# Kernel optimization log

Measured on AMD Instinct MI355X. Metric: run time of the kernel, lower is better.

## Reference

```python
import jax, jax.numpy as jnp
import numpy as np

N = 100000       # nodes
E = 1600000      # edges
DIM_IN = 128
DIM_H = 256
G = 512          # graphs in batch


def setup_inputs() -> dict:
    key = jax.random.key(0)
    ks = jax.random.split(key, 9)
    x = jax.random.normal(ks[0], (N, DIM_IN), dtype=jnp.float32)
    edge_index = jax.random.randint(ks[1], (2, E), 0, N, dtype=jnp.int32)
    batch = jnp.sort(jax.random.randint(ks[2], (N,), 0, G, dtype=jnp.int32))
    # GCNConv weights (glorot-ish scale) + biases, and linear head
    W1 = jax.random.normal(ks[3], (DIM_IN, DIM_H), dtype=jnp.float32) / np.sqrt(DIM_IN)
    b1 = jnp.zeros((DIM_H,), dtype=jnp.float32)
    W2 = jax.random.normal(ks[4], (DIM_H, DIM_H), dtype=jnp.float32) / np.sqrt(DIM_H)
    b2 = jnp.zeros((DIM_H,), dtype=jnp.float32)
    Wl = jax.random.normal(ks[5], (DIM_H, 1), dtype=jnp.float32) / np.sqrt(DIM_H)
    bl = jnp.zeros((1,), dtype=jnp.float32)
    return {"x": x, "edge_index": edge_index, "batch": batch,
            "W1": W1, "b1": b1, "W2": W2, "b2": b2, "Wl": Wl, "bl": bl}


def _gcn_conv(x, W, b, src, dst, norm):
    # PyG GCNConv: h = x @ W; message = norm_e * h[src]; aggregate at dst; + bias
    h = x @ W                                  # [N, d_out]
    msg = h[src] * norm[:, None]               # [E+N, d_out] edge-gathered
    out = jax.ops.segment_sum(msg, dst, num_segments=N)
    return out + b


def reference(x, edge_index, batch, W1, b1, W2, b2, Wl, bl):
    # add self-loops (PyG GCNConv default)
    loops = jnp.arange(N, dtype=edge_index.dtype)
    src = jnp.concatenate([edge_index[0], loops])   # [E+N]
    dst = jnp.concatenate([edge_index[1], loops])   # [E+N]
    # symmetric normalization: deg counted at dst (incl. self-loops)
    deg = jax.ops.segment_sum(jnp.ones_like(src, dtype=x.dtype), dst, num_segments=N)
    dinv = jax.lax.rsqrt(deg)                       # deg >= 1 due to self-loops
    norm = dinv[src] * dinv[dst]                    # [E+N]

    h = jax.nn.relu(_gcn_conv(x, W1, b1, src, dst, norm))
    h = jax.nn.relu(_gcn_conv(h, W2, b2, src, dst, norm))

    # global_mean_pool over graph ids
    sums = jax.ops.segment_sum(h, batch, num_segments=G)                  # [G, d]
    cnts = jax.ops.segment_sum(jnp.ones((N,), h.dtype), batch, num_segments=G)
    pooled = sums / jnp.maximum(cnts, 1.0)[:, None]

    return pooled @ Wl + bl                                              # [G, 1]
```

## Files before the change

### kernel.cpp

```cpp
#include <hip/hip_runtime.h>
#include <hip/hip_fp16.h>
#include <math.h>

typedef _Float16 f16x8 __attribute__((ext_vector_type(8)));
typedef float f32x4 __attribute__((ext_vector_type(4)));


__global__ void k_init(int* __restrict__ ecnt, int* __restrict__ cursor, int N) {
    int i = blockIdx.x * 256 + threadIdx.x;
    if (i < N) { ecnt[i] = 0; cursor[i] = 0; }
}

__global__ void k_edge_count(const int* __restrict__ dst, int* __restrict__ ecnt, int E) {
    int i = blockIdx.x * 256 + threadIdx.x;
    if (i < E) atomicAdd(&ecnt[dst[i]], 1);
}

__global__ void k_scanA(const int* __restrict__ ecnt, int* __restrict__ bsum, int N) {
    int t = threadIdx.x;
    int base = blockIdx.x * 1024;
    int s = 0;
#pragma unroll
    for (int j = 0; j < 4; ++j) {
        int i = base + j * 256 + t;
        if (i < N) s += ecnt[i];
    }
#pragma unroll
    for (int off = 32; off > 0; off >>= 1) s += __shfl_down(s, off, 64);
    __shared__ int wsum[4];
    if ((t & 63) == 0) wsum[t >> 6] = s;
    __syncthreads();
    if (t == 0) bsum[blockIdx.x] = wsum[0] + wsum[1] + wsum[2] + wsum[3];
}

__global__ void k_scanB(const int* __restrict__ bsum, int* __restrict__ boff, int NB) {
    __shared__ int sh[256];
    int t = threadIdx.x;
    int v = (t < NB) ? bsum[t] : 0;
    sh[t] = v;
    __syncthreads();
    for (int off = 1; off < 256; off <<= 1) {
        int u = (t >= off) ? sh[t - off] : 0;
        __syncthreads();
        sh[t] += u;
        __syncthreads();
    }
    if (t < NB) boff[t] = sh[t] - v;
}

__global__ void k_scanC(const int* __restrict__ ecnt, const int* __restrict__ boff,
                        int* __restrict__ rowstart, float* __restrict__ dinv, int N) {
    int t = threadIdx.x;
    int base = blockIdx.x * 1024 + t * 4;
    int e[4];
    int s = 0;
#pragma unroll
    for (int j = 0; j < 4; ++j) {
        int i = base + j;
        e[j] = (i < N) ? ecnt[i] : 0;
        s += e[j];
    }
    __shared__ int sh[256];
    sh[t] = s;
    __syncthreads();
    for (int off = 1; off < 256; off <<= 1) {
        int u = (t >= off) ? sh[t - off] : 0;
        __syncthreads();
        sh[t] += u;
        __syncthreads();
    }
    int off0 = boff[blockIdx.x] + sh[t] - s;
    int run = 0;
#pragma unroll
    for (int j = 0; j < 4; ++j) {
        int i = base + j;
        if (i < N) {
            rowstart[i] = off0 + run;
            dinv[i] = rsqrtf((float)(e[j] + 1));
        }
        run += e[j];
    }
}

__global__ void k_tail(int* __restrict__ rowstart, int N, int E) {
    rowstart[N] = E;
}

__global__ void k_scatter(const int* __restrict__ src, const int* __restrict__ dst,
                          const int* __restrict__ rowstart, int* __restrict__ cursor,
                          int* __restrict__ ssrc, int E) {
    int i = blockIdx.x * 256 + threadIdx.x;
    if (i < E) {
        int v = dst[i];
        int p = rowstart[v] + atomicAdd(&cursor[v], 1);
        ssrc[p] = src[i];
    }
}

__global__ void k_gstarts(const int* __restrict__ batch, int* __restrict__ gstart, int N, int G) {
    int i = blockIdx.x * 256 + threadIdx.x;
    if (i >= N) return;
    int bi = batch[i];
    int bp = (i == 0) ? -1 : batch[i - 1];
    for (int g = bp + 1; g <= bi; ++g) gstart[g] = i;
    if (i == N - 1) {
        for (int g = bi + 1; g <= G; ++g) gstart[g] = N;
    }
}


__global__ __launch_bounds__(256) void k_cast_f2h(const float* __restrict__ in,
                                                  __half* __restrict__ out, int n4) {
    int i = blockIdx.x * 256 + threadIdx.x;
    if (i >= n4) return;
    float4 v = *(const float4*)(in + (size_t)i * 4);
    __half2 a = __floats2half2_rn(v.x, v.y);
    __half2 b = __floats2half2_rn(v.z, v.w);
    union { __half2 h[2]; float2 f; } u;
    u.h[0] = a; u.h[1] = b;
    *(float2*)(out + (size_t)i * 4) = u.f;
}


__global__ __launch_bounds__(256) void k_wt(const float* __restrict__ W,
                                            _Float16* __restrict__ Wt, int K) {
    int idx = blockIdx.x * 256 + threadIdx.x;
    if (idx >= K * 256) return;
    int c = idx / K, k = idx - c * K;
    Wt[idx] = (_Float16)W[k * 256 + c];
}


__device__ __forceinline__ void acc_h4(float4& acc, float2 raw, float d) {
    union { float2 f; __half2 h[2]; } u;
    u.f = raw;
    float2 p0 = __half22float2(u.h[0]);
    float2 p1 = __half22float2(u.h[1]);
    acc.x = fmaf(p0.x, d, acc.x);
    acc.y = fmaf(p0.y, d, acc.y);
    acc.z = fmaf(p1.x, d, acc.z);
    acc.w = fmaf(p1.y, d, acc.w);
}

__global__ __launch_bounds__(256) void k_agg_in(
    const float* __restrict__ x, const __half* __restrict__ xh,
    const int* __restrict__ rowstart, const int* __restrict__ ssrc,
    const float* __restrict__ dinv, __half* __restrict__ xa_h, int N) {
    int half_id = threadIdx.x >> 5;
    int l = threadIdx.x & 31;
    int v = blockIdx.x * 8 + half_id;
    if (v >= N) return;
    float dv = dinv[v];
    float4 s = *(const float4*)(x + (size_t)v * 128 + l * 4);
    float4 acc = make_float4(s.x * dv, s.y * dv, s.z * dv, s.w * dv);
    int e = rowstart[v], e1 = rowstart[v + 1];
    for (; e + 4 <= e1; e += 4) {
        int u0 = ssrc[e], u1 = ssrc[e + 1], u2 = ssrc[e + 2], u3 = ssrc[e + 3];
        float d0 = dinv[u0], d1 = dinv[u1], d2 = dinv[u2], d3 = dinv[u3];
        float2 m0 = *(const float2*)(xh + (size_t)u0 * 128 + l * 4);
        float2 m1 = *(const float2*)(xh + (size_t)u1 * 128 + l * 4);
        float2 m2 = *(const float2*)(xh + (size_t)u2 * 128 + l * 4);
        float2 m3 = *(const float2*)(xh + (size_t)u3 * 128 + l * 4);
        acc_h4(acc, m0, d0);
        acc_h4(acc, m1, d1);
        acc_h4(acc, m2, d2);
        acc_h4(acc, m3, d3);
    }
    for (; e < e1; ++e) {
        int u = ssrc[e];
        float d = dinv[u];
        float2 m = *(const float2*)(xh + (size_t)u * 128 + l * 4);
        acc_h4(acc, m, d);
    }
    union { __half2 h[2]; float2 f; } uo;
    uo.h[0] = __floats2half2_rn(acc.x * dv, acc.y * dv);
    uo.h[1] = __floats2half2_rn(acc.z * dv, acc.w * dv);
    *(float2*)(xa_h + (size_t)v * 128 + l * 4) = uo.f;
}


__device__ __forceinline__ void acc_h4s(float4& acc, float2 raw) {
    union { float2 f; __half2 h[2]; } u;
    u.f = raw;
    float2 p0 = __half22float2(u.h[0]);
    float2 p1 = __half22float2(u.h[1]);
    acc.x += p0.x; acc.y += p0.y; acc.z += p1.x; acc.w += p1.y;
}

__global__ __launch_bounds__(256) void k_aggregate(
    const __half* __restrict__ hsh, const int* __restrict__ rowstart,
    const int* __restrict__ ssrc, const float* __restrict__ dinv,
    const float* __restrict__ bias, float* __restrict__ out, int N) {
    int w = threadIdx.x >> 6;
    int l = threadIdx.x & 63;
    int v = blockIdx.x * 4 + w;
    if (v >= N) return;
    float4 acc = make_float4(0.f, 0.f, 0.f, 0.f);
    acc_h4s(acc, *(const float2*)(hsh + (size_t)v * 256 + l * 4));
    int e = rowstart[v], e1 = rowstart[v + 1];
    for (; e + 4 <= e1; e += 4) {
        int u0 = ssrc[e], u1 = ssrc[e + 1], u2 = ssrc[e + 2], u3 = ssrc[e + 3];
        float2 m0 = *(const float2*)(hsh + (size_t)u0 * 256 + l * 4);
        float2 m1 = *(const float2*)(hsh + (size_t)u1 * 256 + l * 4);
        float2 m2 = *(const float2*)(hsh + (size_t)u2 * 256 + l * 4);
        float2 m3 = *(const float2*)(hsh + (size_t)u3 * 256 + l * 4);
        acc_h4s(acc, m0);
        acc_h4s(acc, m1);
        acc_h4s(acc, m2);
        acc_h4s(acc, m3);
    }
    for (; e < e1; ++e) {
        int u = ssrc[e];
        acc_h4s(acc, *(const float2*)(hsh + (size_t)u * 256 + l * 4));
    }
    float d = dinv[v];
    float4 b = *(const float4*)(bias + l * 4);
    float4 o;
    o.x = fmaxf(fmaf(acc.x, d, b.x), 0.f);
    o.y = fmaxf(fmaf(acc.y, d, b.y), 0.f);
    o.z = fmaxf(fmaf(acc.z, d, b.z), 0.f);
    o.w = fmaxf(fmaf(acc.w, d, b.w), 0.f);
    *(float4*)(out + (size_t)v * 256 + l * 4) = o;
}


template<int K, int EPI>
__global__ __launch_bounds__(256, 2) void k_gemm_mfma(
    const _Float16* __restrict__ Ah, const _Float16* __restrict__ Wt,
    const float* __restrict__ dinv, const float* __restrict__ bias,
    _Float16* __restrict__ Ch, int Nrows, int nchunks) {
    constexpr int KS = K / 32;
    constexpr int RB = 2 * K;
    constexpr int NLD = 64 * RB / 4096;
    __shared__ _Float16 As[64 * K];

    int tid = threadIdx.x;
    int l = tid & 63;
    int wv = tid >> 6;

    int bc = wv * 64 + (l & 15);
    int bk = (l >> 4) * 8;
    f16x8 breg[4][KS];
#pragma unroll
    for (int ct = 0; ct < 4; ++ct)
#pragma unroll
        for (int ks = 0; ks < KS; ++ks)
            breg[ct][ks] = *(const f16x8*)(Wt + (size_t)(bc + ct * 16) * K + ks * 32 + bk);
    float bb[4];
    if (EPI == 1) {
#pragma unroll
        for (int ct = 0; ct < 4; ++ct) bb[ct] = bias[bc + ct * 16];
    }

    for (int ch = blockIdx.x; ch < nchunks; ch += gridDim.x) {
        int r0 = ch * 64;
#pragma unroll
        for (int i = 0; i < NLD; ++i) {
            int logical = i * 4096 + tid * 16;
            int row = logical / RB;
            int colb = (logical & (RB - 1)) ^ ((row & 7) << 4);
            int grow = r0 + row;
            grow = grow < Nrows ? grow : Nrows - 1;
            const char* src = (const char*)Ah + (size_t)grow * RB + colb;
            char* dst = (char*)As + i * 4096 + wv * 1024;
            __builtin_amdgcn_global_load_lds(
                (const __attribute__((address_space(1))) void*)src,
                (__attribute__((address_space(3))) void*)dst, 16, 0, 0);
        }
        __syncthreads();

#pragma unroll
        for (int rb = 0; rb < 4; ++rb) {
            f32x4 acc[4];
#pragma unroll
            for (int ct = 0; ct < 4; ++ct) acc[ct] = (f32x4){0.f, 0.f, 0.f, 0.f};
            int row = rb * 16 + (l & 15);
#pragma unroll
            for (int ks = 0; ks < KS; ++ks) {
                int lb = (row * RB + ks * 64 + (l >> 4) * 16) ^ ((l & 7) << 4);
                f16x8 a = *(const f16x8*)((const char*)As + lb);
#pragma unroll
                for (int ct = 0; ct < 4; ++ct)
                    acc[ct] = __builtin_amdgcn_mfma_f32_16x16x32_f16(a, breg[ct][ks], acc[ct], 0, 0, 0);
            }
            int rbase = r0 + rb * 16 + (l >> 4) * 4;
#pragma unroll
            for (int j = 0; j < 4; ++j) {
                int r = rbase + j;
                if (r < Nrows) {
                    if (EPI == 0) {
                        float sc = dinv[r];
#pragma unroll
                        for (int ct = 0; ct < 4; ++ct)
                            Ch[(size_t)r * 256 + bc + ct * 16] = (_Float16)(acc[ct][j] * sc);
                    } else {
#pragma unroll
                        for (int ct = 0; ct < 4; ++ct)
                            Ch[(size_t)r * 256 + bc + ct * 16] =
                                (_Float16)fmaxf(acc[ct][j] + bb[ct], 0.f);
                    }
                }
            }
        }
        __syncthreads();
    }
}


__global__ __launch_bounds__(256) void k_pool_head(
    const float* __restrict__ h2, const int* __restrict__ gstart,
    const float* __restrict__ Wl, const float* __restrict__ bl,
    float* __restrict__ out, int G) {
    int g = blockIdx.x;
    int t = threadIdx.x;
    int i0 = gstart[g], i1 = gstart[g + 1];
    float s = 0.f;
    for (int i = i0; i < i1; ++i) s += h2[(size_t)i * 256 + t];
    float cnt = (float)(i1 - i0);
    float pooled = s / fmaxf(cnt, 1.f);
    float v = pooled * Wl[t];
#pragma unroll
    for (int off = 32; off > 0; off >>= 1) v += __shfl_down(v, off, 64);
    __shared__ float red[4];
    if ((t & 63) == 0) red[t >> 6] = v;
    __syncthreads();
    if (t == 0) out[g] = red[0] + red[1] + red[2] + red[3] + bl[0];
}


extern "C" void kernel_launch(void* const* d_in, const int* in_sizes, int n_in,
                              void* d_out, int out_size, void* d_ws, size_t ws_size,
                              hipStream_t stream) {
    const float* x  = (const float*)d_in[0];
    const int* ei   = (const int*)d_in[1];
    const int* batch= (const int*)d_in[2];
    const float* W1 = (const float*)d_in[3];
    const float* b1 = (const float*)d_in[4];
    const float* W2 = (const float*)d_in[5];
    const float* b2 = (const float*)d_in[6];
    const float* Wl = (const float*)d_in[7];
    const float* bl = (const float*)d_in[8];
    float* out = (float*)d_out;

    const int N = in_sizes[2];
    const int E = in_sizes[1] / 2;
    const int G = out_size;

    char* wsp = (char*)d_ws;
    size_t off = 0;
    auto carve = [&](size_t bytes) -> void* {
        void* p = wsp + off;
        off = (off + bytes + 255) & ~(size_t)255;
        return p;
    };
    float* bufA    = (float*)carve((size_t)N * 256 * 4);
    float* bufB    = (float*)carve((size_t)N * 256 * 4);
    float* dinv    = (float*)carve((size_t)N * 4);
    int* ecnt      = (int*)carve((size_t)N * 4);
    int* rowstart  = (int*)carve((size_t)(N + 1) * 4);
    int* cursor    = (int*)carve((size_t)N * 4);
    int* ssrc      = (int*)carve((size_t)E * 4);
    const int NB = (N + 1023) / 1024;
    int* bsum      = (int*)carve((size_t)NB * 4);
    int* boff      = (int*)carve((size_t)NB * 4);
    int* gstart    = (int*)carve((size_t)(G + 1) * 4);
    _Float16* W1t  = (_Float16*)carve((size_t)256 * 128 * 2);
    _Float16* W2t  = (_Float16*)carve((size_t)256 * 256 * 2);
    (void)ws_size;

    __half*    xh   = (__half*)bufA;
    __half*    xa_h = (__half*)((char*)bufA + (size_t)N * 128 * 2);
    _Float16*  h1h  = (_Float16*)((char*)bufA + (size_t)N * 128 * 4);
    _Float16*  hsh  = (_Float16*)bufB;
    float*     h2   = bufA;

    const int* esrc = ei;
    const int* edst = ei + E;

    int nb256 = (N + 255) / 256;
    int eb256 = (E + 255) / 256;
    int nchunks = (N + 63) / 64;

    hipLaunchKernelGGL(k_init, dim3(nb256), dim3(256), 0, stream, ecnt, cursor, N);
    hipLaunchKernelGGL(k_edge_count, dim3(eb256), dim3(256), 0, stream, edst, ecnt, E);
    hipLaunchKernelGGL(k_scanA, dim3(NB), dim3(256), 0, stream, ecnt, bsum, N);
    hipLaunchKernelGGL(k_scanB, dim3(1), dim3(256), 0, stream, bsum, boff, NB);
    hipLaunchKernelGGL(k_scanC, dim3(NB), dim3(256), 0, stream, ecnt, boff, rowstart, dinv, N);
    hipLaunchKernelGGL(k_tail, dim3(1), dim3(1), 0, stream, rowstart, N, E);
    hipLaunchKernelGGL(k_scatter, dim3(eb256), dim3(256), 0, stream, esrc, edst, rowstart, cursor, ssrc, E);
    hipLaunchKernelGGL(k_gstarts, dim3(nb256), dim3(256), 0, stream, batch, gstart, N, G);
    hipLaunchKernelGGL(k_cast_f2h, dim3((N * 32 + 255) / 256), dim3(256), 0, stream,
                       x, xh, N * 32);
    hipLaunchKernelGGL(k_wt, dim3(128), dim3(256), 0, stream, W1, W1t, 128);
    hipLaunchKernelGGL(k_wt, dim3(256), dim3(256), 0, stream, W2, W2t, 256);

    hipLaunchKernelGGL(k_agg_in, dim3((N + 7) / 8), dim3(256), 0, stream,
                       x, xh, rowstart, ssrc, dinv, xa_h, N);
    hipLaunchKernelGGL((k_gemm_mfma<128, 1>), dim3(512), dim3(256), 0, stream,
                       (const _Float16*)xa_h, W1t, (const float*)nullptr, b1, h1h, N, nchunks);
    hipLaunchKernelGGL((k_gemm_mfma<256, 0>), dim3(512), dim3(256), 0, stream,
                       h1h, W2t, dinv, (const float*)nullptr, hsh, N, nchunks);
    hipLaunchKernelGGL(k_aggregate, dim3((N + 3) / 4), dim3(256), 0, stream,
                       (const __half*)hsh, rowstart, ssrc, dinv, b2, h2, N);
    hipLaunchKernelGGL(k_pool_head, dim3(G), dim3(256), 0, stream, h2, gstart, Wl, bl, out, G);
}
```

Measured before the change: 493.2 us.

## Fuse second aggregation with mean pooling, widen gathers, merge tiny kernels

```diff
diff --git a/kernel.cpp b/kernel.cpp
--- a/kernel.cpp
+++ b/kernel.cpp
@@ -12,8 +12,14 @@
 }
 
 __global__ void k_edge_count(const int* __restrict__ dst, int* __restrict__ ecnt, int E) {
-    int i = blockIdx.x * 256 + threadIdx.x;
-    if (i < E) atomicAdd(&ecnt[dst[i]], 1);
+    int j = (blockIdx.x * 256 + threadIdx.x) * 2;
+    if (j + 1 < E) {
+        int2 d = *(const int2*)(dst + j);
+        atomicAdd(&ecnt[d.x], 1);
+        atomicAdd(&ecnt[d.y], 1);
+    } else if (j < E) {
+        atomicAdd(&ecnt[dst[j]], 1);
+    }
 }
 
 __global__ void k_scanA(const int* __restrict__ ecnt, int* __restrict__ bsum, int N) {
@@ -33,7 +39,8 @@
     if (t == 0) bsum[blockIdx.x] = wsum[0] + wsum[1] + wsum[2] + wsum[3];
 }
 
-__global__ void k_scanB(const int* __restrict__ bsum, int* __restrict__ boff, int NB) {
+__global__ void k_scanB(const int* __restrict__ bsum, int* __restrict__ boff, int NB,
+                        int* __restrict__ rowstart, int N, int E) {
     __shared__ int sh[256];
     int t = threadIdx.x;
     int v = (t < NB) ? bsum[t] : 0;
@@ -46,6 +53,7 @@
         __syncthreads();
     }
     if (t < NB) boff[t] = sh[t] - v;
+    if (t == 0) rowstart[N] = E;
 }
 
 __global__ void k_scanC(const int* __restrict__ ecnt, const int* __restrict__ boff,
@@ -82,23 +90,28 @@
     }
 }
 
-__global__ void k_tail(int* __restrict__ rowstart, int N, int E) {
-    rowstart[N] = E;
-}
-
 __global__ void k_scatter(const int* __restrict__ src, const int* __restrict__ dst,
                           const int* __restrict__ rowstart, int* __restrict__ cursor,
                           int* __restrict__ ssrc, int E) {
+    int j = (blockIdx.x * 256 + threadIdx.x) * 2;
+    if (j + 1 < E) {
+        int2 s = *(const int2*)(src + j);
+        int2 d = *(const int2*)(dst + j);
+        int p0 = rowstart[d.x] + atomicAdd(&cursor[d.x], 1);
+        ssrc[p0] = s.x;
+        int p1 = rowstart[d.y] + atomicAdd(&cursor[d.y], 1);
+        ssrc[p1] = s.y;
+    } else if (j < E) {
+        int v = dst[j];
+        int p = rowstart[v] + atomicAdd(&cursor[v], 1);
+        ssrc[p] = src[j];
+    }
+}
+
+__global__ void k_gstarts(const int* __restrict__ batch, int* __restrict__ gstart,
+                          float* __restrict__ pooled, int N, int G) {
     int i = blockIdx.x * 256 + threadIdx.x;
-    if (i < E) {
-        int v = dst[i];
-        int p = rowstart[v] + atomicAdd(&cursor[v], 1);
-        ssrc[p] = src[i];
-    }
-}
-
-__global__ void k_gstarts(const int* __restrict__ batch, int* __restrict__ gstart, int N, int G) {
-    int i = blockIdx.x * 256 + threadIdx.x;
+    if (i < G * 256) pooled[i] = 0.f;
     if (i >= N) return;
     int bi = batch[i];
     int bp = (i == 0) ? -1 : batch[i - 1];
@@ -131,96 +144,115 @@
 }
 
 
-__device__ __forceinline__ void acc_h4(float4& acc, float2 raw, float d) {
-    union { float2 f; __half2 h[2]; } u;
-    u.f = raw;
-    float2 p0 = __half22float2(u.h[0]);
-    float2 p1 = __half22float2(u.h[1]);
-    acc.x = fmaf(p0.x, d, acc.x);
-    acc.y = fmaf(p0.y, d, acc.y);
-    acc.z = fmaf(p1.x, d, acc.z);
-    acc.w = fmaf(p1.y, d, acc.w);
-}
-
 __global__ __launch_bounds__(256) void k_agg_in(
-    const float* __restrict__ x, const __half* __restrict__ xh,
+    const float* __restrict__ x, const _Float16* __restrict__ xh,
     const int* __restrict__ rowstart, const int* __restrict__ ssrc,
-    const float* __restrict__ dinv, __half* __restrict__ xa_h, int N) {
-    int half_id = threadIdx.x >> 5;
-    int l = threadIdx.x & 31;
-    int v = blockIdx.x * 8 + half_id;
+    const float* __restrict__ dinv, _Float16* __restrict__ xa_h, int N) {
+    int qw = threadIdx.x >> 4;
+    int l = threadIdx.x & 15;
+    int v = blockIdx.x * 16 + qw;
     if (v >= N) return;
     float dv = dinv[v];
-    float4 s = *(const float4*)(x + (size_t)v * 128 + l * 4);
-    float4 acc = make_float4(s.x * dv, s.y * dv, s.z * dv, s.w * dv);
+    float acc[8];
+    {
+        float4 s0 = *(const float4*)(x + (size_t)v * 128 + l * 8);
+        float4 s1 = *(const float4*)(x + (size_t)v * 128 + l * 8 + 4);
+        acc[0] = s0.x * dv; acc[1] = s0.y * dv; acc[2] = s0.z * dv; acc[3] = s0.w * dv;
+        acc[4] = s1.x * dv; acc[5] = s1.y * dv; acc[6] = s1.z * dv; acc[7] = s1.w * dv;
+    }
     int e = rowstart[v], e1 = rowstart[v + 1];
     for (; e + 4 <= e1; e += 4) {
         int u0 = ssrc[e], u1 = ssrc[e + 1], u2 = ssrc[e + 2], u3 = ssrc[e + 3];
         float d0 = dinv[u0], d1 = dinv[u1], d2 = dinv[u2], d3 = dinv[u3];
-        float2 m0 = *(const float2*)(xh + (size_t)u0 * 128 + l * 4);
-        float2 m1 = *(const float2*)(xh + (size_t)u1 * 128 + l * 4);
-        float2 m2 = *(const float2*)(xh + (size_t)u2 * 128 + l * 4);
-        float2 m3 = *(const float2*)(xh + (size_t)u3 * 128 + l * 4);
-        acc_h4(acc, m0, d0);
-        acc_h4(acc, m1, d1);
-        acc_h4(acc, m2, d2);
-        acc_h4(acc, m3, d3);
+        f16x8 m0 = *(const f16x8*)(xh + (size_t)u0 * 128 + l * 8);
+        f16x8 m1 = *(const f16x8*)(xh + (size_t)u1 * 128 + l * 8);
+        f16x8 m2 = *(const f16x8*)(xh + (size_t)u2 * 128 + l * 8);
+        f16x8 m3 = *(const f16x8*)(xh + (size_t)u3 * 128 + l * 8);
+#pragma unroll
+        for (int j = 0; j < 8; ++j) {
+            acc[j] = fmaf((float)m0[j], d0, acc[j]);
+            acc[j] = fmaf((float)m1[j], d1, acc[j]);
+            acc[j] = fmaf((float)m2[j], d2, acc[j]);
+            acc[j] = fmaf((float)m3[j], d3, acc[j]);
+        }
     }
     for (; e < e1; ++e) {
         int u = ssrc[e];
         float d = dinv[u];
-        float2 m = *(const float2*)(xh + (size_t)u * 128 + l * 4);
-        acc_h4(acc, m, d);
-    }
-    union { __half2 h[2]; float2 f; } uo;
-    uo.h[0] = __floats2half2_rn(acc.x * dv, acc.y * dv);
-    uo.h[1] = __floats2half2_rn(acc.z * dv, acc.w * dv);
-    *(float2*)(xa_h + (size_t)v * 128 + l * 4) = uo.f;
-}
-
-
-__device__ __forceinline__ void acc_h4s(float4& acc, float2 raw) {
-    union { float2 f; __half2 h[2]; } u;
-    u.f = raw;
-    float2 p0 = __half22float2(u.h[0]);
-    float2 p1 = __half22float2(u.h[1]);
-    acc.x += p0.x; acc.y += p0.y; acc.z += p1.x; acc.w += p1.y;
-}
-
-__global__ __launch_bounds__(256) void k_aggregate(
-    const __half* __restrict__ hsh, const int* __restrict__ rowstart,
+        f16x8 m = *(const f16x8*)(xh + (size_t)u * 128 + l * 8);
+#pragma unroll
+        for (int j = 0; j < 8; ++j) acc[j] = fmaf((float)m[j], d, acc[j]);
+    }
+    f16x8 o;
+#pragma unroll
+    for (int j = 0; j < 8; ++j) o[j] = (_Float16)(acc[j] * dv);
+    *(f16x8*)(xa_h + (size_t)v * 128 + l * 8) = o;
+}
+
+
+__global__ __launch_bounds__(256) void k_aggpool(
+    const _Float16* __restrict__ hsh, const int* __restrict__ rowstart,
     const int* __restrict__ ssrc, const float* __restrict__ dinv,
-    const float* __restrict__ bias, float* __restrict__ out, int N) {
-    int w = threadIdx.x >> 6;
-    int l = threadIdx.x & 63;
-    int v = blockIdx.x * 4 + w;
-    if (v >= N) return;
-    float4 acc = make_float4(0.f, 0.f, 0.f, 0.f);
-    acc_h4s(acc, *(const float2*)(hsh + (size_t)v * 256 + l * 4));
-    int e = rowstart[v], e1 = rowstart[v + 1];
-    for (; e + 4 <= e1; e += 4) {
-        int u0 = ssrc[e], u1 = ssrc[e + 1], u2 = ssrc[e + 2], u3 = ssrc[e + 3];
-        float2 m0 = *(const float2*)(hsh + (size_t)u0 * 256 + l * 4);
-        float2 m1 = *(const float2*)(hsh + (size_t)u1 * 256 + l * 4);
-        float2 m2 = *(const float2*)(hsh + (size_t)u2 * 256 + l * 4);
-        float2 m3 = *(const float2*)(hsh + (size_t)u3 * 256 + l * 4);
-        acc_h4s(acc, m0);
-        acc_h4s(acc, m1);
-        acc_h4s(acc, m2);
-        acc_h4s(acc, m3);
-    }
-    for (; e < e1; ++e) {
-        int u = ssrc[e];
-        acc_h4s(acc, *(const float2*)(hsh + (size_t)u * 256 + l * 4));
-    }
-    float d = dinv[v];
-    float4 b = *(const float4*)(bias + l * 4);
-    float4 o;
-    o.x = fmaxf(fmaf(acc.x, d, b.x), 0.f);
-    o.y = fmaxf(fmaf(acc.y, d, b.y), 0.f);
-    o.z = fmaxf(fmaf(acc.z, d, b.z), 0.f);
-    o.w = fmaxf(fmaf(acc.w, d, b.w), 0.f);
-    *(float4*)(out + (size_t)v * 256 + l * 4) = o;
+    const float* __restrict__ bias, const int* __restrict__ batch,
+    float* __restrict__ pooled, int N) {
+    int hw = threadIdx.x >> 5;
+    int l = threadIdx.x & 31;
+    int n0 = (blockIdx.x * 8 + hw) * 8;
+    if (n0 >= N) return;
+    int n1 = n0 + 8 < N ? n0 + 8 : N;
+
+    float b8[8];
+#pragma unroll
+    for (int j = 0; j < 8; ++j) b8[j] = bias[l * 8 + j];
+
+    float accg[8] = {0.f, 0.f, 0.f, 0.f, 0.f, 0.f, 0.f, 0.f};
+    int curg = -1;
+
+    for (int n = n0; n < n1; ++n) {
+        float acc[8];
+        {
+            f16x8 s = *(const f16x8*)(hsh + (size_t)n * 256 + l * 8);
+#pragma unroll
+            for (int j = 0; j < 8; ++j) acc[j] = (float)s[j];
+        }
+        int e = rowstart[n], e1 = rowstart[n + 1];
+        for (; e + 4 <= e1; e += 4) {
+            int u0 = ssrc[e], u1 = ssrc[e + 1], u2 = ssrc[e + 2], u3 = ssrc[e + 3];
+            f16x8 m0 = *(const f16x8*)(hsh + (size_t)u0 * 256 + l * 8);
+            f16x8 m1 = *(const f16x8*)(hsh + (size_t)u1 * 256 + l * 8);
+            f16x8 m2 = *(const f16x8*)(hsh + (size_t)u2 * 256 + l * 8);
+            f16x8 m3 = *(const f16x8*)(hsh + (size_t)u3 * 256 + l * 8);
+#pragma unroll
+            for (int j = 0; j < 8; ++j)
+                acc[j] += (float)m0[j] + (float)m1[j] + (float)m2[j] + (float)m3[j];
+        }
+        for (; e < e1; ++e) {
+            int u = ssrc[e];
+            f16x8 m = *(const f16x8*)(hsh + (size_t)u * 256 + l * 8);
+#pragma unroll
+            for (int j = 0; j < 8; ++j) acc[j] += (float)m[j];
+        }
+        float d = dinv[n];
+        int g = batch[n];
+        if (g != curg) {
+            if (curg >= 0) {
+#pragma unroll
+                for (int j = 0; j < 8; ++j)
+                    atomicAdd(&pooled[(size_t)curg * 256 + l * 8 + j], accg[j]);
+            }
+            curg = g;
+#pragma unroll
+            for (int j = 0; j < 8; ++j) accg[j] = 0.f;
+        }
+#pragma unroll
+        for (int j = 0; j < 8; ++j)
+            accg[j] += fmaxf(fmaf(acc[j], d, b8[j]), 0.f);
+    }
+    if (curg >= 0) {
+#pragma unroll
+        for (int j = 0; j < 8; ++j)
+            atomicAdd(&pooled[(size_t)curg * 256 + l * 8 + j], accg[j]);
+    }
 }
 
 
@@ -307,24 +339,23 @@
 }
 
 
-__global__ __launch_bounds__(256) void k_pool_head(
-    const float* __restrict__ h2, const int* __restrict__ gstart,
+__global__ __launch_bounds__(256) void k_head(
+    const float* __restrict__ pooled, const int* __restrict__ gstart,
     const float* __restrict__ Wl, const float* __restrict__ bl,
     float* __restrict__ out, int G) {
-    int g = blockIdx.x;
-    int t = threadIdx.x;
-    int i0 = gstart[g], i1 = gstart[g + 1];
+    int g = blockIdx.x * 4 + (threadIdx.x >> 6);
+    int l = threadIdx.x & 63;
+    if (g >= G) return;
+    float cnt = fmaxf((float)(gstart[g + 1] - gstart[g]), 1.f);
     float s = 0.f;
-    for (int i = i0; i < i1; ++i) s += h2[(size_t)i * 256 + t];
-    float cnt = (float)(i1 - i0);
-    float pooled = s / fmaxf(cnt, 1.f);
-    float v = pooled * Wl[t];
-#pragma unroll
-    for (int off = 32; off > 0; off >>= 1) v += __shfl_down(v, off, 64);
-    __shared__ float red[4];
-    if ((t & 63) == 0) red[t >> 6] = v;
-    __syncthreads();
-    if (t == 0) out[g] = red[0] + red[1] + red[2] + red[3] + bl[0];
+#pragma unroll
+    for (int j = 0; j < 4; ++j) {
+        int c = l * 4 + j;
+        s = fmaf(pooled[(size_t)g * 256 + c], Wl[c], s);
+    }
+#pragma unroll
+    for (int off = 32; off > 0; off >>= 1) s += __shfl_down(s, off, 64);
+    if (l == 0) out[g] = s / cnt + bl[0];
 }
 
 
@@ -366,41 +397,43 @@
     int* gstart    = (int*)carve((size_t)(G + 1) * 4);
     _Float16* W1t  = (_Float16*)carve((size_t)256 * 128 * 2);
     _Float16* W2t  = (_Float16*)carve((size_t)256 * 256 * 2);
+    float* pooled  = (float*)carve((size_t)G * 256 * 4);
     (void)ws_size;
 
-    __half*    xh   = (__half*)bufA;
-    __half*    xa_h = (__half*)((char*)bufA + (size_t)N * 128 * 2);
-    _Float16*  h1h  = (_Float16*)((char*)bufA + (size_t)N * 128 * 4);
-    _Float16*  hsh  = (_Float16*)bufB;
-    float*     h2   = bufA;
+    _Float16* xh   = (_Float16*)bufA;
+    _Float16* xa_h = (_Float16*)((char*)bufA + (size_t)N * 128 * 2);
+    _Float16* h1h  = (_Float16*)((char*)bufA + (size_t)N * 128 * 4);
+    _Float16* hsh  = (_Float16*)bufB;
 
     const int* esrc = ei;
     const int* edst = ei + E;
 
     int nb256 = (N + 255) / 256;
-    int eb256 = (E + 255) / 256;
     int nchunks = (N + 63) / 64;
+    int gzb = (G * 256 + 255) / 256;
+    int gsblocks = gzb > nb256 ? gzb : nb256;
 
     hipLaunchKernelGGL(k_init, dim3(nb256), dim3(256), 0, stream, ecnt, cursor, N);
-    hipLaunchKernelGGL(k_edge_count, dim3(eb256), dim3(256), 0, stream, edst, ecnt, E);
+    hipLaunchKernelGGL(k_edge_count, dim3((E / 2 + 255) / 256), dim3(256), 0, stream, edst, ecnt, E);
     hipLaunchKernelGGL(k_scanA, dim3(NB), dim3(256), 0, stream, ecnt, bsum, N);
-    hipLaunchKernelGGL(k_scanB, dim3(1), dim3(256), 0, stream, bsum, boff, NB);
+    hipLaunchKernelGGL(k_scanB, dim3(1), dim3(256), 0, stream, bsum, boff, NB, rowstart, N, E);
     hipLaunchKernelGGL(k_scanC, dim3(NB), dim3(256), 0, stream, ecnt, boff, rowstart, dinv, N);
-    hipLaunchKernelGGL(k_tail, dim3(1), dim3(1), 0, stream, rowstart, N, E);
-    hipLaunchKernelGGL(k_scatter, dim3(eb256), dim3(256), 0, stream, esrc, edst, rowstart, cursor, ssrc, E);
-    hipLaunchKernelGGL(k_gstarts, dim3(nb256), dim3(256), 0, stream, batch, gstart, N, G);
+    hipLaunchKernelGGL(k_scatter, dim3((E / 2 + 255) / 256), dim3(256), 0, stream,
+                       esrc, edst, rowstart, cursor, ssrc, E);
+    hipLaunchKernelGGL(k_gstarts, dim3(gsblocks), dim3(256), 0, stream, batch, gstart, pooled, N, G);
     hipLaunchKernelGGL(k_cast_f2h, dim3((N * 32 + 255) / 256), dim3(256), 0, stream,
-                       x, xh, N * 32);
+                       x, (__half*)xh, N * 32);
     hipLaunchKernelGGL(k_wt, dim3(128), dim3(256), 0, stream, W1, W1t, 128);
     hipLaunchKernelGGL(k_wt, dim3(256), dim3(256), 0, stream, W2, W2t, 256);
 
-    hipLaunchKernelGGL(k_agg_in, dim3((N + 7) / 8), dim3(256), 0, stream,
+    hipLaunchKernelGGL(k_agg_in, dim3((N + 15) / 16), dim3(256), 0, stream,
                        x, xh, rowstart, ssrc, dinv, xa_h, N);
     hipLaunchKernelGGL((k_gemm_mfma<128, 1>), dim3(512), dim3(256), 0, stream,
-                       (const _Float16*)xa_h, W1t, (const float*)nullptr, b1, h1h, N, nchunks);
+                       xa_h, W1t, (const float*)nullptr, b1, h1h, N, nchunks);
     hipLaunchKernelGGL((k_gemm_mfma<256, 0>), dim3(512), dim3(256), 0, stream,
                        h1h, W2t, dinv, (const float*)nullptr, hsh, N, nchunks);
-    hipLaunchKernelGGL(k_aggregate, dim3((N + 3) / 4), dim3(256), 0, stream,
-                       (const __half*)hsh, rowstart, ssrc, dinv, b2, h2, N);
-    hipLaunchKernelGGL(k_pool_head, dim3(G), dim3(256), 0, stream, h2, gstart, Wl, bl, out, G);
-}
+    hipLaunchKernelGGL(k_aggpool, dim3((N + 63) / 64), dim3(256), 0, stream,
+                       hsh, rowstart, ssrc, dinv, b2, batch, pooled, N);
+    hipLaunchKernelGGL(k_head, dim3((G + 3) / 4), dim3(256), 0, stream,
+                       pooled, gstart, Wl, bl, out, G);
+}
```

Result: slower. 529.3 us (+7.3%).
